# Optimization experiments

Hardware: AMD Instinct MI355X
Metric: run time of the kernel (lower is better)

## Reference

```python
import jax, jax.numpy as jnp
import numpy as np

EMBED = 1024
HEADS = 16
HEAD_DIM = EMBED // HEADS


def setup_inputs() -> dict:
    key = jax.random.key(0)
    ks = jax.random.split(key, 10)
    N, S, D = 2, 2048, EMBED
    scale = 1.0 / np.sqrt(D)
    inp = {
        "x": jax.random.normal(ks[0], (N, S, D), dtype=jnp.float32),
        "mask": jax.random.randint(ks[1], (N, 1, S, S), 0, 2, dtype=jnp.int32),
        "Wq": jax.random.normal(ks[2], (D, D), dtype=jnp.float32) * scale,
        "bq": jnp.zeros((D,), dtype=jnp.float32),
        "Wk": jax.random.normal(ks[3], (D, D), dtype=jnp.float32) * scale,
        "bk": jnp.zeros((D,), dtype=jnp.float32),
        "Wv": jax.random.normal(ks[4], (D, D), dtype=jnp.float32) * scale,
        "bv": jnp.zeros((D,), dtype=jnp.float32),
        "Wo": jax.random.normal(ks[5], (D, D), dtype=jnp.float32) * scale,
        "bo": jnp.zeros((D,), dtype=jnp.float32),
    }
    return inp


def reference(x, mask, Wq, bq, Wk, bk, Wv, bv, Wo, bo):
    N, S, D = x.shape
    H, Hd = HEADS, HEAD_DIM
    def split_heads(t):
        return t.reshape(N, S, H, Hd).transpose(0, 2, 1, 3)  # [N,H,S,Hd]
    q = split_heads(x @ Wq + bq)
    k = split_heads(x @ Wk + bk)
    v = split_heads(x @ Wv + bv)
    scores = jnp.einsum("nhqd,nhkd->nhqk", q, k) / jnp.sqrt(jnp.float32(Hd))
    scores = jnp.where(mask == 0, jnp.float32(-jnp.inf), scores)
    attn = jax.nn.softmax(scores, axis=-1)
    out = jnp.einsum("nhqk,nhkd->nhqd", attn, v)
    out = out.transpose(0, 2, 1, 3).reshape(N, S, D)
    return out @ Wo + bo
```

## Files before the change

### kernel.cpp

```cpp
#include <hip/hip_runtime.h>
#include <stdint.h>


typedef _Float16 h8 __attribute__((ext_vector_type(8)));
typedef _Float16 h4 __attribute__((ext_vector_type(4)));
typedef float f32x4 __attribute__((ext_vector_type(4)));

#define MFMA16(a, b, c) __builtin_amdgcn_mfma_f32_16x16x32_f16(a, b, c, 0, 0, 0)

static __device__ __forceinline__ int swz128(int row, int colB) {
    return (row * 128 + colB) ^ ((row & 7) << 4);
}

__global__ __launch_bounds__(256) void k_pack_mask(const int* __restrict__ mask,
                                                   uint32_t* __restrict__ mp) {
    int i = blockIdx.x * 256 + threadIdx.x;
    unsigned long long b = __ballot(mask[i] != 0);
    if ((threadIdx.x & 63) == 0) {
        *(unsigned long long*)(mp + (i >> 5)) = b;
    }
}

__global__ __launch_bounds__(256) void k_wt(const float* __restrict__ W0,
                                            const float* __restrict__ W1,
                                            const float* __restrict__ W2,
                                            _Float16* __restrict__ out) {
    const int nb = blockIdx.x, kb = blockIdx.y, z = blockIdx.z;
    const float* W = (z == 0) ? W0 : ((z == 1) ? W1 : W2);
    _Float16* O = out + (size_t)z * 1024 * 1024;
    __shared__ __align__(16) _Float16 lds[64][68];
    const int t = threadIdx.x;
    const int k0 = kb * 64, n0 = nb * 64;
#pragma unroll
    for (int p = 0; p < 4; ++p) {
        int idx = t + p * 256;
        int kr = idx >> 4;
        int c = idx & 15;
        float4 v = *(const float4*)(W + (size_t)(k0 + kr) * 1024 + n0 + c * 4);
        h4 hv;
        hv[0] = (_Float16)v.x; hv[1] = (_Float16)v.y;
        hv[2] = (_Float16)v.z; hv[3] = (_Float16)v.w;
        *(h4*)(&lds[kr][c * 4]) = hv;
    }
    __syncthreads();
#pragma unroll
    for (int p = 0; p < 2; ++p) {
        int idx = t + p * 256;
        int n = idx >> 3;
        int kc = idx & 7;
        h8 o;
#pragma unroll
        for (int i = 0; i < 8; ++i) o[i] = lds[kc * 8 + i][n];
        *(h8*)(O + (size_t)(n0 + n) * 1024 + k0 + kc * 8) = o;
    }
}

__global__ __launch_bounds__(256) void k_qkv(const float* __restrict__ X,
                                             const _Float16* __restrict__ Wt,
                                             const float* __restrict__ bq,
                                             const float* __restrict__ bk,
                                             const float* __restrict__ bv,
                                             _Float16* __restrict__ Qo,
                                             _Float16* __restrict__ Ko,
                                             _Float16* __restrict__ Vo) {
    const int nt = blockIdx.x;
    const int mt = blockIdx.y;
    const int z = blockIdx.z;
    const _Float16* W = Wt + (size_t)z * 1024 * 1024;
    const float* bias = (z == 0) ? bq : ((z == 1) ? bk : bv);
    _Float16* Out = (z == 0) ? Qo : ((z == 1) ? Ko : Vo);

    __shared__ __align__(16) char lds[32768];
    char* As = lds;
    char* Bs = lds + 16384;

    const int t = threadIdx.x;
    const int lane = t & 63;
    const int w = t >> 6;
    const int wm = w >> 1, wn = w & 1;
    const int m0 = mt * 128, n0 = nt * 128;

    f32x4 acc[4][4] = {};

    for (int kt = 0; kt < 16; ++kt) {
        const int k0 = kt * 64;
#pragma unroll
        for (int p = 0; p < 8; ++p) {
            int idx = t + p * 256;
            int row = idx >> 4;
            int c4 = idx & 15;
            float4 v = *(const float4*)(X + (size_t)(m0 + row) * 1024 + k0 + c4 * 4);
            h4 hv;
            hv[0] = (_Float16)v.x; hv[1] = (_Float16)v.y;
            hv[2] = (_Float16)v.z; hv[3] = (_Float16)v.w;
            *(h4*)(As + swz128(row, c4 * 8)) = hv;
        }
#pragma unroll
        for (int p = 0; p < 4; ++p) {
            int idx = t + p * 256;
            int row = idx >> 3;
            int c = idx & 7;
            uint4 v = *(const uint4*)(W + (size_t)(n0 + row) * 1024 + k0 + c * 8);
            *(uint4*)(Bs + swz128(row, c * 16)) = v;
        }
        __syncthreads();

#pragma unroll
        for (int kk = 0; kk < 2; ++kk) {
            h8 af[4], bf[4];
#pragma unroll
            for (int fm = 0; fm < 4; ++fm)
                af[fm] = *(h8*)(As + swz128(wm * 64 + fm * 16 + (lane & 15),
                                            kk * 64 + (lane >> 4) * 16));
#pragma unroll
            for (int fn = 0; fn < 4; ++fn)
                bf[fn] = *(h8*)(Bs + swz128(wn * 64 + fn * 16 + (lane & 15),
                                            kk * 64 + (lane >> 4) * 16));
#pragma unroll
            for (int fm = 0; fm < 4; ++fm)
#pragma unroll
                for (int fn = 0; fn < 4; ++fn)
                    acc[fm][fn] = MFMA16(af[fm], bf[fn], acc[fm][fn]);
        }
        __syncthreads();
    }

#pragma unroll
    for (int fn = 0; fn < 4; ++fn) {
        int n = n0 + wn * 64 + fn * 16 + (lane & 15);
        float bv_ = bias[n];
        int h = n >> 6, d = n & 63;
#pragma unroll
        for (int fm = 0; fm < 4; ++fm) {
#pragma unroll
            for (int r = 0; r < 4; ++r) {
                int m = m0 + wm * 64 + fm * 16 + (lane >> 4) * 4 + r;
                int bi = m >> 11, s = m & 2047;
                float val = acc[fm][fn][r] + bv_;
                Out[(size_t)((bi * 16 + h) * 2048 + s) * 64 + d] = (_Float16)val;
            }
        }
    }
}

__global__ __launch_bounds__(256) void k_vt(const _Float16* __restrict__ V,
                                            _Float16* __restrict__ Vt) {
    const int st = blockIdx.x;
    const int nh = blockIdx.y;
    __shared__ __align__(16) _Float16 lds[64][80];
    const int t = threadIdx.x;
    {
        int r = t >> 2;
#pragma unroll
        for (int p = 0; p < 2; ++p) {
            int c = (t & 3) + p * 4;
            h8 v = *(const h8*)(V + ((size_t)nh * 2048 + st * 64 + r) * 64 + c * 8);
            *(h8*)(&lds[r][c * 8]) = v;
        }
    }
    __syncthreads();
    {
        int d = t >> 2;
#pragma unroll
        for (int p = 0; p < 2; ++p) {
            int c = (t & 3) + p * 4;
            h8 o;
#pragma unroll
            for (int i = 0; i < 8; ++i) o[i] = lds[c * 8 + i][d];
            *(h8*)(Vt + ((size_t)nh * 64 + d) * 2048 + st * 64 + c * 8) = o;
        }
    }
}

__global__ __launch_bounds__(256) void k_attn(const _Float16* __restrict__ Q,
                                              const _Float16* __restrict__ K,
                                              const _Float16* __restrict__ Vt,
                                              const uint32_t* __restrict__ mp,
                                              _Float16* __restrict__ ctx) {
    const int qt = blockIdx.x;
    const int nh = blockIdx.y;
    const int bi = nh >> 4;
    const int t = threadIdx.x, lane = t & 63, w = t >> 6;

    __shared__ __align__(16) char lds[32768];
    char* Ks = lds;
    char* Vs = lds + 8192;
    char* Ps = lds + 16384 + w * 4096;

    const int qbase = qt * 128 + w * 32;
    const int qr4 = (lane >> 4) * 4;

    h8 qf[2][2];
#pragma unroll
    for (int rf = 0; rf < 2; ++rf)
#pragma unroll
        for (int kk = 0; kk < 2; ++kk)
            qf[rf][kk] = *(const h8*)(Q + ((size_t)nh * 2048 + qbase + rf * 16 + (lane & 15)) * 64 +
                                      kk * 32 + (lane >> 4) * 8);

    f32x4 of[2][4] = {};
    float lrow[2][4] = {};

    const size_t kbase = (size_t)nh * 2048 * 64;
    const size_t vbase = (size_t)nh * 64 * 2048;
    const float C1 = 0.18033688f;
    const float C2 = 11.541560f;

    for (int kt = 0; kt < 32; ++kt) {
#pragma unroll
        for (int p = 0; p < 2; ++p) {
            int c = t + p * 256;
            int row = c >> 3;
            int cb = (c & 7) * 16;
            uint4 kv = *(const uint4*)(K + kbase + (size_t)kt * 4096 + c * 8);
            *(uint4*)(Ks + swz128(row, cb)) = kv;
            uint4 vv = *(const uint4*)(Vt + vbase + (size_t)row * 2048 + kt * 64 + (c & 7) * 8);
            *(uint4*)(Vs + swz128(row, cb)) = vv;
        }
        __syncthreads();

        f32x4 sf[2][4];
#pragma unroll
        for (int fn = 0; fn < 4; ++fn) {
            f32x4 a0 = {}, a1 = {};
#pragma unroll
            for (int kk = 0; kk < 2; ++kk) {
                h8 b = *(h8*)(Ks + swz128(fn * 16 + (lane & 15), kk * 64 + (lane >> 4) * 16));
                a0 = MFMA16(qf[0][kk], b, a0);
                a1 = MFMA16(qf[1][kk], b, a1);
            }
            sf[0][fn] = a0;
            sf[1][fn] = a1;
        }

#pragma unroll
        for (int rf = 0; rf < 2; ++rf) {
#pragma unroll
            for (int r = 0; r < 4; ++r) {
                int s = qbase + rf * 16 + qr4 + r;
                uint2 mw = *(const uint2*)(mp + ((size_t)bi * 2048 + s) * 64 + kt * 2);
                float lacc = 0.f;
#pragma unroll
                for (int fn = 0; fn < 4; ++fn) {
                    uint32_t word = (fn & 2) ? mw.y : mw.x;
                    int bit = ((fn & 1) << 4) + (lane & 15);
                    float p = ((word >> bit) & 1u)
                                  ? __builtin_amdgcn_exp2f(fmaf(sf[rf][fn][r], C1, -C2))
                                  : 0.f;
                    *(_Float16*)(Ps + swz128(rf * 16 + qr4 + r, (fn * 16 + (lane & 15)) * 2)) =
                        (_Float16)p;
                    lacc += p;
                }
                lrow[rf][r] += lacc;
            }
        }

        h8 pa[2][2];
#pragma unroll
        for (int rf = 0; rf < 2; ++rf)
#pragma unroll
            for (int kk = 0; kk < 2; ++kk)
                pa[rf][kk] = *(h8*)(Ps + swz128(rf * 16 + (lane & 15), kk * 64 + (lane >> 4) * 16));
#pragma unroll
        for (int fn = 0; fn < 4; ++fn) {
#pragma unroll
            for (int kk = 0; kk < 2; ++kk) {
                h8 b = *(h8*)(Vs + swz128(fn * 16 + (lane & 15), kk * 64 + (lane >> 4) * 16));
                of[0][fn] = MFMA16(pa[0][kk], b, of[0][fn]);
                of[1][fn] = MFMA16(pa[1][kk], b, of[1][fn]);
            }
        }
        __syncthreads();
    }

#pragma unroll
    for (int rf = 0; rf < 2; ++rf)
#pragma unroll
        for (int r = 0; r < 4; ++r) {
            float l = lrow[rf][r];
            l += __shfl_xor(l, 1);
            l += __shfl_xor(l, 2);
            l += __shfl_xor(l, 4);
            l += __shfl_xor(l, 8);
            lrow[rf][r] = l;
        }

#pragma unroll
    for (int rf = 0; rf < 2; ++rf)
#pragma unroll
        for (int fn = 0; fn < 4; ++fn)
#pragma unroll
            for (int r = 0; r < 4; ++r) {
                int srow = qbase + rf * 16 + qr4 + r;
                float val = of[rf][fn][r] / lrow[rf][r];
                ctx[(size_t)(bi * 2048 + srow) * 1024 + (nh & 15) * 64 + fn * 16 + (lane & 15)] =
                    (_Float16)val;
            }
}

__global__ __launch_bounds__(256) void k_oproj(const _Float16* __restrict__ A,
                                               const _Float16* __restrict__ Wot,
                                               const float* __restrict__ bias,
                                               float* __restrict__ out) {
    const int nt = blockIdx.x, mt = blockIdx.y;
    __shared__ __align__(16) char lds[32768];
    char* As = lds;
    char* Bs = lds + 16384;
    const int t = threadIdx.x, lane = t & 63, w = t >> 6;
    const int wm = w >> 1, wn = w & 1;
    const int m0 = mt * 128, n0 = nt * 128;
    f32x4 acc[4][4] = {};

    for (int kt = 0; kt < 16; ++kt) {
        const int k0 = kt * 64;
#pragma unroll
        for (int p = 0; p < 4; ++p) {
            int idx = t + p * 256;
            int row = idx >> 3;
            int c = idx & 7;
            uint4 v = *(const uint4*)(A + (size_t)(m0 + row) * 1024 + k0 + c * 8);
            *(uint4*)(As + swz128(row, c * 16)) = v;
        }
#pragma unroll
        for (int p = 0; p < 4; ++p) {
            int idx = t + p * 256;
            int row = idx >> 3;
            int c = idx & 7;
            uint4 v = *(const uint4*)(Wot + (size_t)(n0 + row) * 1024 + k0 + c * 8);
            *(uint4*)(Bs + swz128(row, c * 16)) = v;
        }
        __syncthreads();

#pragma unroll
        for (int kk = 0; kk < 2; ++kk) {
            h8 af[4], bf[4];
#pragma unroll
            for (int fm = 0; fm < 4; ++fm)
                af[fm] = *(h8*)(As + swz128(wm * 64 + fm * 16 + (lane & 15),
                                            kk * 64 + (lane >> 4) * 16));
#pragma unroll
            for (int fn = 0; fn < 4; ++fn)
                bf[fn] = *(h8*)(Bs + swz128(wn * 64 + fn * 16 + (lane & 15),
                                            kk * 64 + (lane >> 4) * 16));
#pragma unroll
            for (int fm = 0; fm < 4; ++fm)
#pragma unroll
                for (int fn = 0; fn < 4; ++fn)
                    acc[fm][fn] = MFMA16(af[fm], bf[fn], acc[fm][fn]);
        }
        __syncthreads();
    }

#pragma unroll
    for (int fn = 0; fn < 4; ++fn) {
        int n = n0 + wn * 64 + fn * 16 + (lane & 15);
        float b = bias[n];
#pragma unroll
        for (int fm = 0; fm < 4; ++fm) {
#pragma unroll
            for (int r = 0; r < 4; ++r) {
                int m = m0 + wm * 64 + fm * 16 + (lane >> 4) * 4 + r;
                out[(size_t)m * 1024 + n] = acc[fm][fn][r] + b;
            }
        }
    }
}

extern "C" void kernel_launch(void* const* d_in, const int* in_sizes, int n_in,
                              void* d_out, int out_size, void* d_ws, size_t ws_size,
                              hipStream_t stream) {
    const float* x = (const float*)d_in[0];
    const int* mask = (const int*)d_in[1];
    const float* Wq = (const float*)d_in[2];
    const float* bq = (const float*)d_in[3];
    const float* Wk = (const float*)d_in[4];
    const float* bk = (const float*)d_in[5];
    const float* Wv = (const float*)d_in[6];
    const float* bv = (const float*)d_in[7];
    const float* Wo = (const float*)d_in[8];
    const float* bo = (const float*)d_in[9];
    float* out = (float*)d_out;

    char* ws = (char*)d_ws;
    _Float16* Wt = (_Float16*)(ws);
    _Float16* Vt = (_Float16*)(ws);
    _Float16* Wot = (_Float16*)(ws);
    _Float16* Q = (_Float16*)(ws + (8u << 20));
    _Float16* Kb = (_Float16*)(ws + (16u << 20));
    _Float16* V = (_Float16*)(ws + (24u << 20));
    uint32_t* mp = (uint32_t*)(ws + (32u << 20));
    _Float16* ctx = V;

    k_pack_mask<<<(2 * 2048 * 2048) / 256, 256, 0, stream>>>(mask, mp);
    k_wt<<<dim3(16, 16, 3), 256, 0, stream>>>(Wq, Wk, Wv, Wt);
    k_qkv<<<dim3(8, 32, 3), 256, 0, stream>>>(x, Wt, bq, bk, bv, Q, Kb, V);
    k_vt<<<dim3(32, 32), 256, 0, stream>>>(V, Vt);
    k_attn<<<dim3(16, 32), 256, 0, stream>>>(Q, Kb, Vt, mp, ctx);
    k_wt<<<dim3(16, 16, 1), 256, 0, stream>>>(Wo, Wo, Wo, Wot);
    k_oproj<<<dim3(8, 32), 256, 0, stream>>>(ctx, Wot, bo, out);
}
```

Baseline: 281.8 us.

## Fuse V transpose into QKV epilogue and retile attention to 16 rows per wave

The QKV projection now writes V directly in transposed layout with packed 4-element stores, removing the separate V-transpose kernel and its extra global round-trip. The attention kernel is reworked so each wave handles 16 query rows (64 per block, doubling the grid), computes S^T via swapped MFMA operands, and stores P with vector writes. Row sums reduce with fewer shuffles. Workspace buffers are reassigned so ctx, Vt and Wot no longer alias incorrectly. The smaller per-block tile halves K/V reuse per LDS load in exchange for more blocks and lower register/LDS use.

```diff
diff --git a/kernel.cpp b/kernel.cpp
--- a/kernel.cpp
+++ b/kernel.cpp
@@ -62,13 +62,12 @@
                                              const float* __restrict__ bv,
                                              _Float16* __restrict__ Qo,
                                              _Float16* __restrict__ Ko,
-                                             _Float16* __restrict__ Vo) {
+                                             _Float16* __restrict__ VtO) {
     const int nt = blockIdx.x;
     const int mt = blockIdx.y;
     const int z = blockIdx.z;
     const _Float16* W = Wt + (size_t)z * 1024 * 1024;
     const float* bias = (z == 0) ? bq : ((z == 1) ? bk : bv);
-    _Float16* Out = (z == 0) ? Qo : ((z == 1) ? Ko : Vo);
 
     __shared__ __align__(16) char lds[32768];
     char* As = lds;
@@ -125,49 +124,39 @@
         __syncthreads();
     }
 
-#pragma unroll
-    for (int fn = 0; fn < 4; ++fn) {
-        int n = n0 + wn * 64 + fn * 16 + (lane & 15);
-        float bv_ = bias[n];
-        int h = n >> 6, d = n & 63;
-#pragma unroll
-        for (int fm = 0; fm < 4; ++fm) {
-#pragma unroll
-            for (int r = 0; r < 4; ++r) {
-                int m = m0 + wm * 64 + fm * 16 + (lane >> 4) * 4 + r;
-                int bi = m >> 11, s = m & 2047;
-                float val = acc[fm][fn][r] + bv_;
-                Out[(size_t)((bi * 16 + h) * 2048 + s) * 64 + d] = (_Float16)val;
-            }
-        }
-    }
-}
-
-__global__ __launch_bounds__(256) void k_vt(const _Float16* __restrict__ V,
-                                            _Float16* __restrict__ Vt) {
-    const int st = blockIdx.x;
-    const int nh = blockIdx.y;
-    __shared__ __align__(16) _Float16 lds[64][80];
-    const int t = threadIdx.x;
-    {
-        int r = t >> 2;
-#pragma unroll
-        for (int p = 0; p < 2; ++p) {
-            int c = (t & 3) + p * 4;
-            h8 v = *(const h8*)(V + ((size_t)nh * 2048 + st * 64 + r) * 64 + c * 8);
-            *(h8*)(&lds[r][c * 8]) = v;
-        }
-    }
-    __syncthreads();
-    {
-        int d = t >> 2;
-#pragma unroll
-        for (int p = 0; p < 2; ++p) {
-            int c = (t & 3) + p * 4;
-            h8 o;
-#pragma unroll
-            for (int i = 0; i < 8; ++i) o[i] = lds[c * 8 + i][d];
-            *(h8*)(Vt + ((size_t)nh * 64 + d) * 2048 + st * 64 + c * 8) = o;
+    if (z == 2) {
+#pragma unroll
+        for (int fn = 0; fn < 4; ++fn) {
+            int n = n0 + wn * 64 + fn * 16 + (lane & 15);
+            float bv_ = bias[n];
+            int h = n >> 6, d = n & 63;
+#pragma unroll
+            for (int fm = 0; fm < 4; ++fm) {
+                int m_base = m0 + wm * 64 + fm * 16 + (lane >> 4) * 4;
+                int bi = m_base >> 11, s0 = m_base & 2047;
+                h4 pv;
+#pragma unroll
+                for (int r = 0; r < 4; ++r) pv[r] = (_Float16)(acc[fm][fn][r] + bv_);
+                *(h4*)(VtO + ((size_t)((bi * 16 + h) * 64 + d)) * 2048 + s0) = pv;
+            }
+        }
+    } else {
+        _Float16* Out = (z == 0) ? Qo : Ko;
+#pragma unroll
+        for (int fn = 0; fn < 4; ++fn) {
+            int n = n0 + wn * 64 + fn * 16 + (lane & 15);
+            float bv_ = bias[n];
+            int h = n >> 6, d = n & 63;
+#pragma unroll
+            for (int fm = 0; fm < 4; ++fm) {
+#pragma unroll
+                for (int r = 0; r < 4; ++r) {
+                    int m = m0 + wm * 64 + fm * 16 + (lane >> 4) * 4 + r;
+                    int bi = m >> 11, s = m & 2047;
+                    float val = acc[fm][fn][r] + bv_;
+                    Out[(size_t)((bi * 16 + h) * 2048 + s) * 64 + d] = (_Float16)val;
+                }
+            }
         }
     }
 }
@@ -181,25 +170,23 @@
     const int nh = blockIdx.y;
     const int bi = nh >> 4;
     const int t = threadIdx.x, lane = t & 63, w = t >> 6;
-
-    __shared__ __align__(16) char lds[32768];
+    const int g = lane >> 4;
+    const int q15 = lane & 15;
+
+    __shared__ __align__(16) char lds[24576];
     char* Ks = lds;
     char* Vs = lds + 8192;
-    char* Ps = lds + 16384 + w * 4096;
-
-    const int qbase = qt * 128 + w * 32;
-    const int qr4 = (lane >> 4) * 4;
-
-    h8 qf[2][2];
-#pragma unroll
-    for (int rf = 0; rf < 2; ++rf)
-#pragma unroll
-        for (int kk = 0; kk < 2; ++kk)
-            qf[rf][kk] = *(const h8*)(Q + ((size_t)nh * 2048 + qbase + rf * 16 + (lane & 15)) * 64 +
-                                      kk * 32 + (lane >> 4) * 8);
-
-    f32x4 of[2][4] = {};
-    float lrow[2][4] = {};
+    char* Ps = lds + 16384 + w * 2048;
+
+    const int qbase = qt * 64 + w * 16;
+
+    h8 qf[2];
+#pragma unroll
+    for (int kk = 0; kk < 2; ++kk)
+        qf[kk] = *(const h8*)(Q + ((size_t)nh * 2048 + qbase + q15) * 64 + kk * 32 + g * 8);
+
+    f32x4 of[4] = {};
+    float lacc = 0.f;
 
     const size_t kbase = (size_t)nh * 2048 * 64;
     const size_t vbase = (size_t)nh * 64 * 2048;
@@ -219,83 +206,66 @@
         }
         __syncthreads();
 
-        f32x4 sf[2][4];
-#pragma unroll
-        for (int fn = 0; fn < 4; ++fn) {
-            f32x4 a0 = {}, a1 = {};
+        f32x4 sf[4];
+#pragma unroll
+        for (int fn = 0; fn < 4; ++fn) {
+            f32x4 a = {};
 #pragma unroll
             for (int kk = 0; kk < 2; ++kk) {
-                h8 b = *(h8*)(Ks + swz128(fn * 16 + (lane & 15), kk * 64 + (lane >> 4) * 16));
-                a0 = MFMA16(qf[0][kk], b, a0);
-                a1 = MFMA16(qf[1][kk], b, a1);
-            }
-            sf[0][fn] = a0;
-            sf[1][fn] = a1;
-        }
-
-#pragma unroll
-        for (int rf = 0; rf < 2; ++rf) {
-#pragma unroll
-            for (int r = 0; r < 4; ++r) {
-                int s = qbase + rf * 16 + qr4 + r;
-                uint2 mw = *(const uint2*)(mp + ((size_t)bi * 2048 + s) * 64 + kt * 2);
-                float lacc = 0.f;
-#pragma unroll
-                for (int fn = 0; fn < 4; ++fn) {
-                    uint32_t word = (fn & 2) ? mw.y : mw.x;
-                    int bit = ((fn & 1) << 4) + (lane & 15);
-                    float p = ((word >> bit) & 1u)
-                                  ? __builtin_amdgcn_exp2f(fmaf(sf[rf][fn][r], C1, -C2))
+                h8 kf = *(h8*)(Ks + swz128(fn * 16 + q15, kk * 64 + g * 16));
+                a = MFMA16(kf, qf[kk], a);
+            }
+            sf[fn] = a;
+        }
+
+        {
+            uint2 mw = *(const uint2*)(mp + ((size_t)bi * 2048 + qbase + q15) * 64 + kt * 2);
+#pragma unroll
+            for (int fn = 0; fn < 4; ++fn) {
+                uint32_t word = (fn & 2) ? mw.y : mw.x;
+                int bitbase = ((fn & 1) << 4) + g * 4;
+                h4 pv4;
+#pragma unroll
+                for (int r = 0; r < 4; ++r) {
+                    float p = ((word >> (bitbase + r)) & 1u)
+                                  ? __builtin_amdgcn_exp2f(fmaf(sf[fn][r], C1, -C2))
                                   : 0.f;
-                    *(_Float16*)(Ps + swz128(rf * 16 + qr4 + r, (fn * 16 + (lane & 15)) * 2)) =
-                        (_Float16)p;
                     lacc += p;
+                    pv4[r] = (_Float16)p;
                 }
-                lrow[rf][r] += lacc;
-            }
-        }
-
-        h8 pa[2][2];
-#pragma unroll
-        for (int rf = 0; rf < 2; ++rf)
-#pragma unroll
-            for (int kk = 0; kk < 2; ++kk)
-                pa[rf][kk] = *(h8*)(Ps + swz128(rf * 16 + (lane & 15), kk * 64 + (lane >> 4) * 16));
+                *(h4*)(Ps + swz128(q15, (fn * 16 + g * 4) * 2)) = pv4;
+            }
+        }
+
+        h8 pa[2];
+#pragma unroll
+        for (int kk = 0; kk < 2; ++kk)
+            pa[kk] = *(h8*)(Ps + swz128(q15, kk * 64 + g * 16));
 #pragma unroll
         for (int fn = 0; fn < 4; ++fn) {
 #pragma unroll
             for (int kk = 0; kk < 2; ++kk) {
-                h8 b = *(h8*)(Vs + swz128(fn * 16 + (lane & 15), kk * 64 + (lane >> 4) * 16));
-                of[0][fn] = MFMA16(pa[0][kk], b, of[0][fn]);
-                of[1][fn] = MFMA16(pa[1][kk], b, of[1][fn]);
-            }
-        }
-        __syncthreads();
-    }
-
-#pragma unroll
-    for (int rf = 0; rf < 2; ++rf)
-#pragma unroll
-        for (int r = 0; r < 4; ++r) {
-            float l = lrow[rf][r];
-            l += __shfl_xor(l, 1);
-            l += __shfl_xor(l, 2);
-            l += __shfl_xor(l, 4);
-            l += __shfl_xor(l, 8);
-            lrow[rf][r] = l;
-        }
-
-#pragma unroll
-    for (int rf = 0; rf < 2; ++rf)
-#pragma unroll
-        for (int fn = 0; fn < 4; ++fn)
-#pragma unroll
-            for (int r = 0; r < 4; ++r) {
-                int srow = qbase + rf * 16 + qr4 + r;
-                float val = of[rf][fn][r] / lrow[rf][r];
-                ctx[(size_t)(bi * 2048 + srow) * 1024 + (nh & 15) * 64 + fn * 16 + (lane & 15)] =
-                    (_Float16)val;
-            }
+                h8 vb = *(h8*)(Vs + swz128(fn * 16 + q15, kk * 64 + g * 16));
+                of[fn] = MFMA16(pa[kk], vb, of[fn]);
+            }
+        }
+        __syncthreads();
+    }
+
+    lacc += __shfl_xor(lacc, 16);
+    lacc += __shfl_xor(lacc, 32);
+
+#pragma unroll
+    for (int r = 0; r < 4; ++r) {
+        float lq = __shfl(lacc, g * 4 + r);
+        int srow = qbase + g * 4 + r;
+#pragma unroll
+        for (int fn = 0; fn < 4; ++fn) {
+            float val = of[fn][r] / lq;
+            ctx[(size_t)(bi * 2048 + srow) * 1024 + (nh & 15) * 64 + fn * 16 + q15] =
+                (_Float16)val;
+        }
+    }
 }
 
 __global__ __launch_bounds__(256) void k_oproj(const _Float16* __restrict__ A,
@@ -383,19 +353,17 @@
 
     char* ws = (char*)d_ws;
     _Float16* Wt = (_Float16*)(ws);
-    _Float16* Vt = (_Float16*)(ws);
-    _Float16* Wot = (_Float16*)(ws);
+    _Float16* ctx = (_Float16*)(ws);
     _Float16* Q = (_Float16*)(ws + (8u << 20));
     _Float16* Kb = (_Float16*)(ws + (16u << 20));
-    _Float16* V = (_Float16*)(ws + (24u << 20));
+    _Float16* Vt = (_Float16*)(ws + (24u << 20));
+    _Float16* Wot = (_Float16*)(ws + (24u << 20));
     uint32_t* mp = (uint32_t*)(ws + (32u << 20));
-    _Float16* ctx = V;
 
     k_pack_mask<<<(2 * 2048 * 2048) / 256, 256, 0, stream>>>(mask, mp);
     k_wt<<<dim3(16, 16, 3), 256, 0, stream>>>(Wq, Wk, Wv, Wt);
-    k_qkv<<<dim3(8, 32, 3), 256, 0, stream>>>(x, Wt, bq, bk, bv, Q, Kb, V);
-    k_vt<<<dim3(32, 32), 256, 0, stream>>>(V, Vt);
-    k_attn<<<dim3(16, 32), 256, 0, stream>>>(Q, Kb, Vt, mp, ctx);
+    k_qkv<<<dim3(8, 32, 3), 256, 0, stream>>>(x, Wt, bq, bk, bv, Q, Kb, Vt);
+    k_attn<<<dim3(32, 32), 256, 0, stream>>>(Q, Kb, Vt, mp, ctx);
     k_wt<<<dim3(16, 16, 1), 256, 0, stream>>>(Wo, Wo, Wo, Wot);
     k_oproj<<<dim3(8, 32), 256, 0, stream>>>(ctx, Wot, bo, out);
 }
```

After: 291.6 us. 1.03x slower.
